# Kernel optimization log

Hardware: AMD Instinct MI355X
Metric: run time of the kernel (lower is better)

Reference implementation:

```python
import jax, jax.numpy as jnp
import numpy as np

TEMPERATURE = 0.07
BASE_TEMPERATURE = 0.07
N_CLASSES = 360


def setup_inputs() -> dict:
    key = jax.random.key(0)
    k1, k2 = jax.random.split(key)
    B, D = 8192, 256
    features = jax.random.normal(k1, (B, D), dtype=jnp.float32)
    labels = jax.random.randint(k2, (B,), 0, N_CLASSES, dtype=jnp.int64)
    sigma = jnp.ones((1,), dtype=jnp.float32)
    return {"features": features, "labels": labels, "sigma": sigma}


def reference(features, labels, sigma):
    B = features.shape[0]
    labels = labels.reshape(-1, 1)
    # pairwise positive mask [B, B]
    mask = (labels == labels.T).astype(jnp.float32)
    # negated scaled dot products [B, B]
    anchor_dot_contrast = -(features @ features.T) / TEMPERATURE
    logits_max = jax.lax.stop_gradient(jnp.max(anchor_dot_contrast, axis=1, keepdims=True))
    logits = anchor_dot_contrast - logits_max
    # remove self-pairs
    logits_mask = 1.0 - jnp.eye(B, dtype=jnp.float32)
    mask = mask * logits_mask
    exp_logits = jnp.exp(logits)
    negative_mask = logits_mask - mask
    negative_counts = jnp.sum(negative_mask, axis=1, keepdims=True)
    mean_exp_negatives = jnp.sum(exp_logits * negative_mask, axis=1, keepdims=True) / (negative_counts + 1e-8)
    exp_positives_sum = jnp.sum(exp_logits * mask, axis=1, keepdims=True)
    denominator = exp_positives_sum + mean_exp_negatives
    log_prob = logits - jnp.log(denominator)
    mask_pos_pairs = jnp.sum(mask, axis=1)
    mask_pos_pairs = jnp.where(mask_pos_pairs < 1e-6, 1.0, mask_pos_pairs)
    mean_log_prob_pos = jnp.sum(mask * log_prob, axis=1) / mask_pos_pairs
    loss = (TEMPERATURE / BASE_TEMPERATURE) * mean_log_prob_pos
    return jnp.mean(loss)
```

## Files before the change

### kernel.cpp

```cpp
#include <hip/hip_runtime.h>
#include <hip/hip_bf16.h>
#include <math.h>

typedef unsigned int u32;
typedef unsigned short u16;
typedef __bf16 bf16_t;
typedef bf16_t bf16x8 __attribute__((ext_vector_type(8)));
typedef float f32x4 __attribute__((ext_vector_type(4)));

#define B_N 8192
#define D_K 256
#define NCLS 360
#define BM 128
#define BN 64
#define NSPLIT 8
#define COLS (B_N / NSPLIT)
#define NT (COLS / BN)
#define MAXC 61

#define SCALE2 (-20.609929155556627f)
#define LN2 (0.6931471805599453f)
#define INV_T (14.285714285714286f)

__device__ __forceinline__ float fexp2(float x) { return __builtin_amdgcn_exp2f(x); }

__device__ __forceinline__ u16 f2bf(float x) {
  u32 u = __float_as_uint(x);
  u32 r = (u + 0x7fffu + ((u >> 16) & 1u)) >> 16;
  return (u16)r;
}

__device__ __forceinline__ void gl_lds16(const void* g, void* l) {
  __builtin_amdgcn_global_load_lds(
      (const __attribute__((address_space(1))) u32*)g,
      (__attribute__((address_space(3))) u32*)l, 16, 0, 0);
}

__global__ void k_prep(const float* __restrict__ f, u16* __restrict__ fbf,
                       float* __restrict__ out) {
  if (blockIdx.x == 0 && threadIdx.x == 0) out[0] = 0.f;
  int t = blockIdx.x * 256 + threadIdx.x;
  int e4 = t * 4;
  const float4 v = *reinterpret_cast<const float4*>(f + e4);
  ushort4 b;
  b.x = f2bf(v.x); b.y = f2bf(v.y); b.z = f2bf(v.z); b.w = f2bf(v.w);
  *reinterpret_cast<ushort4*>(fbf + e4) = b;
}

__device__ __forceinline__ void stage_tile(const u16* __restrict__ fb, int col0,
                                           u16* buf, int w, int lane) {
#pragma unroll
  for (int it = 0; it < 8; ++it) {
    int lin = (w * 8 + it) * 1024 + lane * 16;
    int row = lin >> 9;
    int c = (lin >> 4) & 31;
    int q = c ^ (row & 7);
    const u16* src = fb + (size_t)(col0 + row) * D_K + q * 8;
    u16* dst = buf + (w * 8 + it) * 512;
    gl_lds16(src, dst);
  }
}

__global__ __launch_bounds__(256, 2) void k_main(const u16* __restrict__ fb,
                                                 float2* __restrict__ part) {
  __shared__ __align__(16) u16 Bs[2][BN * D_K];

  const int tid = threadIdx.x;
  const int lane = tid & 63;
  const int w = tid >> 6;
  const int t15 = lane & 15;
  const int g = lane >> 4;
  const int t7 = t15 & 7;
  const int rb = blockIdx.x & 63;
  const int sp = blockIdx.x >> 6;
  const int rowbase = rb * BM + w * 32;
  const int colbase = sp * COLS;

  bf16x8 A[2][8];
#pragma unroll
  for (int rs = 0; rs < 2; ++rs)
#pragma unroll
    for (int kk = 0; kk < 8; ++kk) {
      const u16* p = fb + (size_t)(rowbase + rs * 16 + t15) * D_K + kk * 32 + g * 8;
      A[rs][kk] = *reinterpret_cast<const bf16x8*>(p);
    }

  float m2[8], Ea[8];
#pragma unroll
  for (int i = 0; i < 8; ++i) { m2[i] = -1e30f; Ea[i] = 0.f; }

  stage_tile(fb, colbase, &Bs[0][0], w, lane);
  __syncthreads();

  for (int t = 0; t < NT; ++t) {
    if (t + 1 < NT) stage_tile(fb, colbase + (t + 1) * BN, &Bs[(t + 1) & 1][0], w, lane);

    const u16* bufp = &Bs[t & 1][0];
    f32x4 C[2][4];
    const f32x4 z4 = {0.f, 0.f, 0.f, 0.f};
#pragma unroll
    for (int rs = 0; rs < 2; ++rs)
#pragma unroll
      for (int s = 0; s < 4; ++s) C[rs][s] = z4;

#pragma unroll
    for (int kk = 0; kk < 8; ++kk) {
      bf16x8 Bf[4];
#pragma unroll
      for (int s = 0; s < 4; ++s) {
        int rowB = s * 16 + t15;
        int q = (kk * 4 + g) ^ t7;
        Bf[s] = *reinterpret_cast<const bf16x8*>(bufp + rowB * D_K + q * 8);
      }
#pragma unroll
      for (int rs = 0; rs < 2; ++rs)
#pragma unroll
        for (int s = 0; s < 4; ++s)
          C[rs][s] = __builtin_amdgcn_mfma_f32_16x16x32_bf16(A[rs][kk], Bf[s],
                                                             C[rs][s], 0, 0, 0);
    }

#pragma unroll
    for (int rs = 0; rs < 2; ++rs) {
#pragma unroll
      for (int q = 0; q < 4; ++q) {
        const int slot = rs * 4 + q;
        float c0 = C[rs][0][q], c1 = C[rs][1][q];
        float c2 = C[rs][2][q], c3 = C[rs][3][q];
        float tm = fminf(fminf(c0, c1), fminf(c2, c3));
        float nm = fmaxf(m2[slot], tm * SCALE2);
        float sc = fexp2(m2[slot] - nm);
        float e0 = fexp2(fmaf(c0, SCALE2, -nm));
        float e1 = fexp2(fmaf(c1, SCALE2, -nm));
        float e2 = fexp2(fmaf(c2, SCALE2, -nm));
        float e3 = fexp2(fmaf(c3, SCALE2, -nm));
        Ea[slot] = fmaf(Ea[slot], sc, (e0 + e1) + (e2 + e3));
        m2[slot] = nm;
      }
    }
    __syncthreads();
  }

#pragma unroll
  for (int st = 1; st < 16; st <<= 1) {
#pragma unroll
    for (int i = 0; i < 8; ++i) {
      float om = __shfl_xor(m2[i], st);
      float oa = __shfl_xor(Ea[i], st);
      float nm = fmaxf(m2[i], om);
      Ea[i] = Ea[i] * fexp2(m2[i] - nm) + oa * fexp2(om - nm);
      m2[i] = nm;
    }
  }
  if (t15 == 0) {
#pragma unroll
    for (int rs = 0; rs < 2; ++rs)
#pragma unroll
      for (int q = 0; q < 4; ++q) {
        int row = rowbase + rs * 16 + g * 4 + q;
        part[sp * B_N + row] = make_float2(m2[rs * 4 + q], Ea[rs * 4 + q]);
      }
  }
}

__global__ __launch_bounds__(256) void k_final(const float* __restrict__ f,
                                               const int* __restrict__ lab,
                                               const float2* __restrict__ part,
                                               float* __restrict__ out) {
  __shared__ __align__(16) float4 feat[MAXC][65];
  __shared__ float m2a[MAXC], Eaa[MAXC], Epa[MAXC], sda[MAXC];
  __shared__ int idx[MAXC];
  __shared__ int nS;
  const int c = blockIdx.x;
  const int tid = threadIdx.x;
  const int lane = tid & 63;
  const int w = tid >> 6;
  if (tid == 0) nS = 0;
  __syncthreads();

  for (int i = tid; i < B_N / 4; i += 256) {
    const int4 lv = reinterpret_cast<const int4*>(lab)[i];
    if (lv.x == c) { int p = atomicAdd(&nS, 1); if (p < MAXC) idx[p] = i * 4 + 0; }
    if (lv.y == c) { int p = atomicAdd(&nS, 1); if (p < MAXC) idx[p] = i * 4 + 1; }
    if (lv.z == c) { int p = atomicAdd(&nS, 1); if (p < MAXC) idx[p] = i * 4 + 2; }
    if (lv.w == c) { int p = atomicAdd(&nS, 1); if (p < MAXC) idx[p] = i * 4 + 3; }
  }
  __syncthreads();
  const int n = nS < MAXC ? nS : MAXC;

  for (int j = w; j < n; j += 4)
    feat[j][lane] = reinterpret_cast<const float4*>(f + (size_t)idx[j] * D_K)[lane];

  for (int j = w; j < n; j += 4) {
    float m2 = -1e30f, Ea = 0.f;
    if (lane < NSPLIT) {
      float2 p = part[lane * B_N + idx[j]];
      m2 = p.x; Ea = p.y;
    }
#pragma unroll
    for (int st = 1; st < NSPLIT; st <<= 1) {
      float om = __shfl_xor(m2, st);
      float oa = __shfl_xor(Ea, st);
      float nm = fmaxf(m2, om);
      Ea = Ea * fexp2(m2 - nm) + oa * fexp2(om - nm);
      m2 = nm;
    }
    if (lane == 0) { m2a[j] = m2; Eaa[j] = Ea; Epa[j] = 0.f; sda[j] = 0.f; }
  }
  __syncthreads();

  const int ntile = (n + 7) >> 3;
  const int jj = lane >> 3, kk = lane & 7;
  for (int tile = w; tile < ntile * ntile; tile += 4) {
    const int j = (tile / ntile) * 8 + jj;
    const int k = (tile % ntile) * 8 + kk;
    const bool ok = (j < n) && (k < n) && (j != k);
    const int jc = j < n ? j : 0, kc = k < n ? k : 0;
    f32x4 acc = {0.f, 0.f, 0.f, 0.f};
#pragma unroll 8
    for (int d = 0; d < 64; ++d) {
      const float4 a = feat[jc][d];
      const float4 b = feat[kc][d];
      acc[0] = fmaf(a.x, b.x, acc[0]);
      acc[1] = fmaf(a.y, b.y, acc[1]);
      acc[2] = fmaf(a.z, b.z, acc[2]);
      acc[3] = fmaf(a.w, b.w, acc[3]);
    }
    float dot = ok ? ((acc[0] + acc[1]) + (acc[2] + acc[3])) : 0.f;
    float ex = ok ? fexp2(fmaf(dot, SCALE2, -m2a[jc])) : 0.f;
#pragma unroll
    for (int st = 1; st < 8; st <<= 1) {
      dot += __shfl_xor(dot, st);
      ex += __shfl_xor(ex, st);
    }
    if (kk == 0 && j < n) {
      atomicAdd(&sda[j], dot);
      atomicAdd(&Epa[j], ex);
    }
  }
  __syncthreads();

  if (w == 0) {
    float contrib = 0.f;
    if (lane < n) {
      const int j = lane;
      float m2 = m2a[j], Ea = Eaa[j], Ep = Epa[j], sumdot = sda[j];
      float En = fmaxf(Ea - Ep, 0.f);
      int cntp = n - 1;
      float cntn = (float)(B_N - 1 - cntp);
      float denom = Ep + En / (cntn + 1e-8f);
      float Sadc = -sumdot * INV_T;
      float num = Sadc - (float)cntp * (m2 * LN2) - (float)cntp * logf(denom);
      float dv = (cntp <= 0) ? 1.f : (float)cntp;
      contrib = num / dv;
    }
#pragma unroll
    for (int st = 1; st < 64; st <<= 1) contrib += __shfl_xor(contrib, st);
    if (lane == 0) atomicAdd(out, contrib * (1.f / (float)B_N));
  }
}

extern "C" void kernel_launch(void* const* d_in, const int* in_sizes, int n_in,
                              void* d_out, int out_size, void* d_ws, size_t ws_size,
                              hipStream_t stream) {
  const float* f = (const float*)d_in[0];
  const int* lab = (const int*)d_in[1];

  char* ws = (char*)d_ws;
  u16* fbf = (u16*)ws;
  float2* part = (float2*)(ws + 4194304);

  k_prep<<<2048, 256, 0, stream>>>(f, fbf, (float*)d_out);
  k_main<<<64 * NSPLIT, 256, 0, stream>>>(fbf, part);
  k_final<<<NCLS, 256, 0, stream>>>(f, lab, part, (float*)d_out);
}
```

Before: 71.37 us.

## Split K-staging into halves to shrink LDS and double column splits

Stages each B tile in two K-halves of 128 instead of the full 256-wide row, halving the shared-memory buffer. This allows four blocks per CU (launch bounds 4) and doubles the column split count to 16, so more blocks are in flight. The cost is twice as many barriers and stage issues per tile, plus more partial results to combine.

```diff
diff --git a/kernel.cpp b/kernel.cpp
--- a/kernel.cpp
+++ b/kernel.cpp
@@ -13,7 +13,8 @@
 #define NCLS 360
 #define BM 128
 #define BN 64
-#define NSPLIT 8
+#define BKH 128
+#define NSPLIT 16
 #define COLS (B_N / NSPLIT)
 #define NT (COLS / BN)
 #define MAXC 61
@@ -47,23 +48,23 @@
   *reinterpret_cast<ushort4*>(fbf + e4) = b;
 }
 
-__device__ __forceinline__ void stage_tile(const u16* __restrict__ fb, int col0,
-                                           u16* buf, int w, int lane) {
-#pragma unroll
-  for (int it = 0; it < 8; ++it) {
-    int lin = (w * 8 + it) * 1024 + lane * 16;
-    int row = lin >> 9;
-    int c = (lin >> 4) & 31;
-    int q = c ^ (row & 7);
-    const u16* src = fb + (size_t)(col0 + row) * D_K + q * 8;
-    u16* dst = buf + (w * 8 + it) * 512;
+__device__ __forceinline__ void stage_half(const u16* __restrict__ fb, int col0,
+                                           int koff, u16* buf, int w, int lane) {
+#pragma unroll
+  for (int it = 0; it < 4; ++it) {
+    int lin = (w * 4 + it) * 1024 + lane * 16;
+    int row = lin >> 8;
+    int c = (lin >> 4) & 15;
+    int sc = c ^ (row & 7);
+    const u16* src = fb + (size_t)(col0 + row) * D_K + koff + sc * 8;
+    u16* dst = buf + (w * 4 + it) * 512;
     gl_lds16(src, dst);
   }
 }
 
-__global__ __launch_bounds__(256, 2) void k_main(const u16* __restrict__ fb,
+__global__ __launch_bounds__(256, 4) void k_main(const u16* __restrict__ fb,
                                                  float2* __restrict__ part) {
-  __shared__ __align__(16) u16 Bs[2][BN * D_K];
+  __shared__ __align__(16) u16 Bs[2][BN * BKH];
 
   const int tid = threadIdx.x;
   const int lane = tid & 63;
@@ -89,53 +90,60 @@
 #pragma unroll
   for (int i = 0; i < 8; ++i) { m2[i] = -1e30f; Ea[i] = 0.f; }
 
-  stage_tile(fb, colbase, &Bs[0][0], w, lane);
-  __syncthreads();
-
-  for (int t = 0; t < NT; ++t) {
-    if (t + 1 < NT) stage_tile(fb, colbase + (t + 1) * BN, &Bs[(t + 1) & 1][0], w, lane);
-
-    const u16* bufp = &Bs[t & 1][0];
-    f32x4 C[2][4];
-    const f32x4 z4 = {0.f, 0.f, 0.f, 0.f};
-#pragma unroll
-    for (int rs = 0; rs < 2; ++rs)
-#pragma unroll
-      for (int s = 0; s < 4; ++s) C[rs][s] = z4;
-
-#pragma unroll
-    for (int kk = 0; kk < 8; ++kk) {
+  stage_half(fb, colbase, 0, &Bs[0][0], w, lane);
+  __syncthreads();
+
+  f32x4 C[2][4];
+  for (int u = 0; u < 2 * NT; ++u) {
+    const int h = u & 1;
+    if (u + 1 < 2 * NT)
+      stage_half(fb, colbase + ((u + 1) >> 1) * BN, ((u + 1) & 1) * BKH,
+                 &Bs[(u + 1) & 1][0], w, lane);
+
+    const u16* bufp = &Bs[u & 1][0];
+    if (h == 0) {
+      const f32x4 z4 = {0.f, 0.f, 0.f, 0.f};
+#pragma unroll
+      for (int rs = 0; rs < 2; ++rs)
+#pragma unroll
+        for (int s = 0; s < 4; ++s) C[rs][s] = z4;
+    }
+
+#pragma unroll
+    for (int kp = 0; kp < 4; ++kp) {
       bf16x8 Bf[4];
 #pragma unroll
       for (int s = 0; s < 4; ++s) {
         int rowB = s * 16 + t15;
-        int q = (kk * 4 + g) ^ t7;
-        Bf[s] = *reinterpret_cast<const bf16x8*>(bufp + rowB * D_K + q * 8);
+        int q = (kp * 4 + g) ^ t7;
+        Bf[s] = *reinterpret_cast<const bf16x8*>(bufp + rowB * BKH + q * 8);
       }
 #pragma unroll
       for (int rs = 0; rs < 2; ++rs)
 #pragma unroll
         for (int s = 0; s < 4; ++s)
-          C[rs][s] = __builtin_amdgcn_mfma_f32_16x16x32_bf16(A[rs][kk], Bf[s],
+          C[rs][s] = __builtin_amdgcn_mfma_f32_16x16x32_bf16(A[rs][h * 4 + kp], Bf[s],
                                                              C[rs][s], 0, 0, 0);
     }
 
-#pragma unroll
-    for (int rs = 0; rs < 2; ++rs) {
-#pragma unroll
-      for (int q = 0; q < 4; ++q) {
-        const int slot = rs * 4 + q;
-        float c0 = C[rs][0][q], c1 = C[rs][1][q];
-        float c2 = C[rs][2][q], c3 = C[rs][3][q];
-        float tm = fminf(fminf(c0, c1), fminf(c2, c3));
-        float nm = fmaxf(m2[slot], tm * SCALE2);
-        float sc = fexp2(m2[slot] - nm);
-        float e0 = fexp2(fmaf(c0, SCALE2, -nm));
-        float e1 = fexp2(fmaf(c1, SCALE2, -nm));
-        float e2 = fexp2(fmaf(c2, SCALE2, -nm));
-        float e3 = fexp2(fmaf(c3, SCALE2, -nm));
-        Ea[slot] = fmaf(Ea[slot], sc, (e0 + e1) + (e2 + e3));
-        m2[slot] = nm;
+    if (h == 1) {
+#pragma unroll
+      for (int rs = 0; rs < 2; ++rs) {
+#pragma unroll
+        for (int q = 0; q < 4; ++q) {
+          const int slot = rs * 4 + q;
+          float c0 = C[rs][0][q], c1 = C[rs][1][q];
+          float c2 = C[rs][2][q], c3 = C[rs][3][q];
+          float tm = fminf(fminf(c0, c1), fminf(c2, c3));
+          float nm = fmaxf(m2[slot], tm * SCALE2);
+          float sc = fexp2(m2[slot] - nm);
+          float e0 = fexp2(fmaf(c0, SCALE2, -nm));
+          float e1 = fexp2(fmaf(c1, SCALE2, -nm));
+          float e2 = fexp2(fmaf(c2, SCALE2, -nm));
+          float e3 = fexp2(fmaf(c3, SCALE2, -nm));
+          Ea[slot] = fmaf(Ea[slot], sc, (e0 + e1) + (e2 + e3));
+          m2[slot] = nm;
+        }
       }
     }
     __syncthreads();
```

Result: slower. 137.2 us (+92.3%).

## Split B tiles into K-halves with four-stage LDS pipeline and vmcnt waits

Applied to the files above, without the earlier changes.

Splits each 64-column B tile into two K-halves and rotates them through four LDS buffers. Staging runs two half-tiles ahead, and fine-grained s_waitcnt vmcnt(4) plus a barrier replace the full __syncthreads wait. Source and destination pointers are precomputed with a new swizzle layout, and s_setprio is raised around the MFMA blocks. The goal is better overlap of global-to-LDS loads with MFMA work; the cost is more complex hand-written synchronization that depends on the exact count of in-flight loads.

```diff
diff --git a/kernel.cpp b/kernel.cpp
--- a/kernel.cpp
+++ b/kernel.cpp
@@ -16,6 +16,7 @@
 #define NSPLIT 8
 #define COLS (B_N / NSPLIT)
 #define NT (COLS / BN)
+#define HB (BN * 128)
 #define MAXC 61
 
 #define SCALE2 (-20.609929155556627f)
@@ -47,23 +48,9 @@
   *reinterpret_cast<ushort4*>(fbf + e4) = b;
 }
 
-__device__ __forceinline__ void stage_tile(const u16* __restrict__ fb, int col0,
-                                           u16* buf, int w, int lane) {
-#pragma unroll
-  for (int it = 0; it < 8; ++it) {
-    int lin = (w * 8 + it) * 1024 + lane * 16;
-    int row = lin >> 9;
-    int c = (lin >> 4) & 31;
-    int q = c ^ (row & 7);
-    const u16* src = fb + (size_t)(col0 + row) * D_K + q * 8;
-    u16* dst = buf + (w * 8 + it) * 512;
-    gl_lds16(src, dst);
-  }
-}
-
 __global__ __launch_bounds__(256, 2) void k_main(const u16* __restrict__ fb,
                                                  float2* __restrict__ part) {
-  __shared__ __align__(16) u16 Bs[2][BN * D_K];
+  __shared__ __align__(16) u16 Bs[4][HB];
 
   const int tid = threadIdx.x;
   const int lane = tid & 63;
@@ -85,61 +72,99 @@
       A[rs][kk] = *reinterpret_cast<const bf16x8*>(p);
     }
 
+  const u16* srcp[4];
+  u16* dstp[4];
+#pragma unroll
+  for (int it = 0; it < 4; ++it) {
+    int lin = (w * 4 + it) * 1024 + lane * 16;
+    int row = lin >> 8;
+    int c = (lin >> 4) & 15;
+    int q = c ^ (row & 7);
+    srcp[it] = fb + (size_t)(colbase + row) * D_K + q * 8;
+    dstp[it] = &Bs[0][0] + (w * 4 + it) * 512;
+  }
+
+  const int gl8 = (g ^ (t7 & 3)) * 8;
+  const int b2 = (t7 >> 2) & 1;
+  const int offE = t15 * 128 + gl8 + b2 * 32;
+  const int offO = t15 * 128 + gl8 + (b2 ^ 1) * 32;
+
   float m2[8], Ea[8];
 #pragma unroll
   for (int i = 0; i < 8; ++i) { m2[i] = -1e30f; Ea[i] = 0.f; }
 
-  stage_tile(fb, colbase, &Bs[0][0], w, lane);
-  __syncthreads();
-
-  for (int t = 0; t < NT; ++t) {
-    if (t + 1 < NT) stage_tile(fb, colbase + (t + 1) * BN, &Bs[(t + 1) & 1][0], w, lane);
-
-    const u16* bufp = &Bs[t & 1][0];
-    f32x4 C[2][4];
-    const f32x4 z4 = {0.f, 0.f, 0.f, 0.f};
-#pragma unroll
-    for (int rs = 0; rs < 2; ++rs)
-#pragma unroll
-      for (int s = 0; s < 4; ++s) C[rs][s] = z4;
-
-#pragma unroll
-    for (int kk = 0; kk < 8; ++kk) {
-      bf16x8 Bf[4];
-#pragma unroll
-      for (int s = 0; s < 4; ++s) {
-        int rowB = s * 16 + t15;
-        int q = (kk * 4 + g) ^ t7;
-        Bf[s] = *reinterpret_cast<const bf16x8*>(bufp + rowB * D_K + q * 8);
-      }
-#pragma unroll
-      for (int rs = 0; rs < 2; ++rs)
-#pragma unroll
-        for (int s = 0; s < 4; ++s)
-          C[rs][s] = __builtin_amdgcn_mfma_f32_16x16x32_bf16(A[rs][kk], Bf[s],
-                                                             C[rs][s], 0, 0, 0);
-    }
-
-#pragma unroll
-    for (int rs = 0; rs < 2; ++rs) {
-#pragma unroll
-      for (int q = 0; q < 4; ++q) {
-        const int slot = rs * 4 + q;
-        float c0 = C[rs][0][q], c1 = C[rs][1][q];
-        float c2 = C[rs][2][q], c3 = C[rs][3][q];
-        float tm = fminf(fminf(c0, c1), fminf(c2, c3));
-        float nm = fmaxf(m2[slot], tm * SCALE2);
-        float sc = fexp2(m2[slot] - nm);
-        float e0 = fexp2(fmaf(c0, SCALE2, -nm));
-        float e1 = fexp2(fmaf(c1, SCALE2, -nm));
-        float e2 = fexp2(fmaf(c2, SCALE2, -nm));
-        float e3 = fexp2(fmaf(c3, SCALE2, -nm));
-        Ea[slot] = fmaf(Ea[slot], sc, (e0 + e1) + (e2 + e3));
-        m2[slot] = nm;
-      }
-    }
-    __syncthreads();
-  }
+  const f32x4 z4 = {0.f, 0.f, 0.f, 0.f};
+  f32x4 C[2][4];
+
+#define STAGE(b)                                                               \
+  {                                                                            \
+    const int so = ((b) >> 1) * (BN * D_K) + ((b) & 1) * 128;                  \
+    const int dofs = ((b) & 3) * HB;                                           \
+    _Pragma("unroll") for (int it = 0; it < 4; ++it)                           \
+        gl_lds16(srcp[it] + so, dstp[it] + dofs);                              \
+  }
+
+#define COMPUTE_HALF(BUFIDX, H, ZERO)                                          \
+  {                                                                            \
+    const u16* bE = &Bs[(BUFIDX)][0] + offE;                                   \
+    const u16* bO = &Bs[(BUFIDX)][0] + offO;                                   \
+    __builtin_amdgcn_s_setprio(1);                                             \
+    _Pragma("unroll") for (int kl = 0; kl < 4; ++kl) {                         \
+      bf16x8 Bf[4];                                                            \
+      _Pragma("unroll") for (int s = 0; s < 4; ++s) {                          \
+        const u16* ba = (kl & 1) ? bO : bE;                                    \
+        Bf[s] = *reinterpret_cast<const bf16x8*>(ba + (kl >> 1) * 64 + s * 2048); \
+      }                                                                        \
+      _Pragma("unroll") for (int rs = 0; rs < 2; ++rs)                         \
+          _Pragma("unroll") for (int s = 0; s < 4; ++s)                        \
+              C[rs][s] = __builtin_amdgcn_mfma_f32_16x16x32_bf16(              \
+                  A[rs][(H) * 4 + kl], Bf[s],                                  \
+                  ((ZERO) && kl == 0) ? z4 : C[rs][s], 0, 0, 0);               \
+    }                                                                          \
+    __builtin_amdgcn_s_setprio(0);                                             \
+  }
+
+#define EPILOGUE()                                                             \
+  {                                                                            \
+    _Pragma("unroll") for (int rs = 0; rs < 2; ++rs) {                         \
+      _Pragma("unroll") for (int q = 0; q < 4; ++q) {                          \
+        const int slot = rs * 4 + q;                                           \
+        float c0 = C[rs][0][q], c1 = C[rs][1][q];                              \
+        float c2 = C[rs][2][q], c3 = C[rs][3][q];                              \
+        float tm = fminf(fminf(c0, c1), fminf(c2, c3));                        \
+        float nm = fmaxf(m2[slot], tm * SCALE2);                               \
+        float sc = fexp2(m2[slot] - nm);                                       \
+        float e0 = fexp2(fmaf(c0, SCALE2, -nm));                               \
+        float e1 = fexp2(fmaf(c1, SCALE2, -nm));                               \
+        float e2 = fexp2(fmaf(c2, SCALE2, -nm));                               \
+        float e3 = fexp2(fmaf(c3, SCALE2, -nm));                               \
+        Ea[slot] = fmaf(Ea[slot], sc, (e0 + e1) + (e2 + e3));                  \
+        m2[slot] = nm;                                                         \
+      }                                                                        \
+    }                                                                          \
+  }
+
+#define WAIT4_BAR() asm volatile("s_waitcnt vmcnt(4)\n\ts_barrier" ::: "memory")
+#define WAIT0_BAR() asm volatile("s_waitcnt vmcnt(0)\n\ts_barrier" ::: "memory")
+
+  STAGE(0);
+  STAGE(1);
+  WAIT4_BAR();
+
+  for (int t = 0; t < NT - 1; ++t) {
+    const int i0 = (2 * t) & 3, i1 = (2 * t + 1) & 3;
+    STAGE(2 * t + 2);
+    COMPUTE_HALF(i0, 0, true);
+    WAIT4_BAR();
+    STAGE(2 * t + 3);
+    COMPUTE_HALF(i1, 1, false);
+    EPILOGUE();
+    WAIT4_BAR();
+  }
+  COMPUTE_HALF(2, 0, true);
+  WAIT0_BAR();
+  COMPUTE_HALF(3, 1, false);
+  EPILOGUE();
 
 #pragma unroll
   for (int st = 1; st < 16; st <<= 1) {
```

Result: slower. 73.37 us (+2.8%).
